# Kernel tuning notes

Measured on AMD Instinct MI355X. Metric: run time of the kernel, lower is better.

## Reference

```python
import jax, jax.numpy as jnp
import numpy as np

N_NODES = 50000
N_EDGES = 1600000
N_GRAPHS = 64


def gcn_conv(x, edge_index, W, b):
    """GCNConv: out = D^{-1/2} (A + I) D^{-1/2} X W + b (symmetric norm, self-loops)."""
    n = x.shape[0]
    src = jnp.concatenate([edge_index[0], jnp.arange(n)])  # add self-loops
    dst = jnp.concatenate([edge_index[1], jnp.arange(n)])
    deg = jax.ops.segment_sum(jnp.ones_like(dst, dtype=x.dtype), dst, num_segments=n)
    dinv = jax.lax.rsqrt(jnp.maximum(deg, 1.0))
    norm = dinv[src] * dinv[dst]                      # [E+N]
    h = x @ W                                          # transform first (smaller gather)
    msg = norm[:, None] * h[src]                       # [E+N, out_dim]
    out = jax.ops.segment_sum(msg, dst, num_segments=n)
    return out + b


def global_mean_pool(x, batch, num_graphs):
    s = jax.ops.segment_sum(x, batch, num_segments=num_graphs)
    cnt = jax.ops.segment_sum(jnp.ones((x.shape[0],), x.dtype), batch, num_segments=num_graphs)
    return s / jnp.maximum(cnt, 1.0)[:, None]


def setup_inputs() -> dict:
    key = jax.random.key(0)
    ks = jax.random.split(key, 6)
    x = jax.random.normal(ks[0], (N_NODES, 256), dtype=jnp.float32)
    edge_index = jax.random.randint(ks[1], (2, N_EDGES), 0, N_NODES, dtype=jnp.int64)
    batch = jnp.sort(jax.random.randint(ks[2], (N_NODES,), 0, N_GRAPHS, dtype=jnp.int64))
    W1 = jax.random.normal(ks[3], (256, 256), dtype=jnp.float32) * (1.0 / np.sqrt(256))
    b1 = jnp.zeros((256,), jnp.float32)
    W2 = jax.random.normal(ks[4], (256, 10), dtype=jnp.float32) * (1.0 / np.sqrt(256))
    b2 = jnp.zeros((10,), jnp.float32)
    return {"x": x, "edge_index": edge_index, "batch": batch,
            "W1": W1, "b1": b1, "W2": W2, "b2": b2}


def reference(x, edge_index, batch, W1, b1, W2, b2):
    h = gcn_conv(x, edge_index, W1, b1)
    h = jax.nn.elu(h)
    # dropout: identity (inference mode, training=False)
    h = gcn_conv(h, edge_index, W2, b2)
    h = jax.nn.elu(h)
    g = global_mean_pool(h, batch, N_GRAPHS)          # [num_graphs, num_class]
    return jax.nn.log_softmax(g, axis=-1)
```

## Files before the change

### kernel.cpp

```cpp
#include <hip/hip_runtime.h>
#include <hip/hip_bf16.h>
#include <math.h>

typedef unsigned int uint;
typedef unsigned short ushort;

typedef __attribute__((ext_vector_type(8))) short bf16x8;
typedef __attribute__((ext_vector_type(4))) float f32x4;

__device__ __forceinline__ float bf2f(uint u) {
    return __uint_as_float(u << 16);
}
__device__ __forceinline__ ushort f2bf(float f) {
    uint u = __float_as_uint(f);
    uint rounding = 0x7fffu + ((u >> 16) & 1u);
    return (ushort)((u + rounding) >> 16);
}
__device__ __forceinline__ float elu(float x) {
    return x > 0.f ? x : expm1f(x);
}

__global__ void count_kernel(const int* __restrict__ dst, int E, int* __restrict__ cnt) {
    int i = blockIdx.x * blockDim.x + threadIdx.x;
    int stride = gridDim.x * blockDim.x;
    for (; i < E; i += stride) atomicAdd(&cnt[dst[i]], 1);
}

__global__ void scan1_kernel(const int* __restrict__ cnt, int NN, int* __restrict__ partials) {
    __shared__ int sh[256];
    int i = blockIdx.x * 256 + threadIdx.x;
    sh[threadIdx.x] = (i < NN) ? cnt[i] : 0;
    __syncthreads();
    for (int s = 128; s > 0; s >>= 1) {
        if (threadIdx.x < s) sh[threadIdx.x] += sh[threadIdx.x + s];
        __syncthreads();
    }
    if (threadIdx.x == 0) partials[blockIdx.x] = sh[0];
}

__global__ void scan2_kernel(const int* __restrict__ partials, int nb, int* __restrict__ pscan) {
    if (threadIdx.x == 0) {
        int run = 0;
        for (int b = 0; b < nb; ++b) { pscan[b] = run; run += partials[b]; }
    }
}

__global__ void scan3_kernel(const int* __restrict__ cnt, int NN, const int* __restrict__ pscan,
                             int* __restrict__ offs, int* __restrict__ cursor,
                             float* __restrict__ dinv) {
    __shared__ int sh[256];
    int t = threadIdx.x;
    int i = blockIdx.x * 256 + t;
    int v = (i < NN) ? cnt[i] : 0;
    sh[t] = v;
    __syncthreads();
    for (int d = 1; d < 256; d <<= 1) {
        int x = (t >= d) ? sh[t - d] : 0;
        __syncthreads();
        sh[t] += x;
        __syncthreads();
    }
    int incl = sh[t];
    int excl = incl - v;
    int base = pscan[blockIdx.x];
    if (i < NN) {
        offs[i]   = base + excl;
        cursor[i] = base + excl;
        dinv[i]   = rsqrtf((float)v + 1.0f);
        if (i == NN - 1) offs[NN] = base + incl;
    }
}

__global__ __launch_bounds__(256) void scatter_kernel(const int* __restrict__ src,
                                                      const int* __restrict__ dst, int E,
                                                      int* __restrict__ cursor,
                                                      int* __restrict__ ssrc, int NN) {
    int grp = blockIdx.x & 7;
    int per = (NN + 7) >> 3;
    int lo = grp * per;
    int hi = min(NN, lo + per);
    int bid = blockIdx.x >> 3;
    int nb  = gridDim.x >> 3;
    int i = bid * blockDim.x + threadIdx.x;
    int stride = nb * blockDim.x;
    for (; i < E; i += stride) {
        int d = dst[i];
        if (d >= lo && d < hi) {
            int pos = atomicAdd(&cursor[d], 1);
            ssrc[pos] = src[i];
        }
    }
}

__global__ void gstart_kernel(const int* __restrict__ batch, int NN, int NG,
                              int* __restrict__ gstart) {
    int g = blockIdx.x * blockDim.x + threadIdx.x;
    if (g > NG) return;
    int lo = 0, hi = NN;
    while (lo < hi) {
        int mid = (lo + hi) >> 1;
        if (batch[mid] < g) lo = mid + 1; else hi = mid;
    }
    gstart[g] = lo;
}

__global__ __launch_bounds__(256) void wtrans_kernel(const float* __restrict__ W,
                                                     ushort* __restrict__ WT) {
    __shared__ float T[64][68];
    int b = blockIdx.x;
    int kt = (b >> 2) * 64, nt = (b & 3) * 64;
    int t = threadIdx.x;
    int r = t >> 4, c4 = (t & 15) * 4;
    #pragma unroll
    for (int h = 0; h < 4; ++h) {
        int rr = r + h * 16;
        float4 v = *reinterpret_cast<const float4*>(&W[(size_t)(kt + rr) * 256 + nt + c4]);
        *reinterpret_cast<float4*>(&T[rr][c4]) = v;
    }
    __syncthreads();
    int nr = t >> 2, ks = (t & 3) * 16;
    uint o[8];
    #pragma unroll
    for (int i = 0; i < 16; i += 2) {
        float f0 = T[ks + i][nr];
        float f1 = T[ks + i + 1][nr];
        o[i >> 1] = (uint)f2bf(f0) | ((uint)f2bf(f1) << 16);
    }
    size_t base = (size_t)(nt + nr) * 256 + kt + ks;
    *reinterpret_cast<uint4*>(&WT[base])     = make_uint4(o[0], o[1], o[2], o[3]);
    *reinterpret_cast<uint4*>(&WT[base + 8]) = make_uint4(o[4], o[5], o[6], o[7]);
}

#define G1_STRIDE 40
__global__ __launch_bounds__(256) void gemm1_mfma_kernel(const float* __restrict__ X,
                                                         const ushort* __restrict__ W1T,
                                                         const float* __restrict__ dinv,
                                                         ushort* __restrict__ H1, int M) {
    __shared__ ushort Xs[64 * G1_STRIDE];
    __shared__ ushort Ws[256 * G1_STRIDE];
    __shared__ float  Dvs[64];
    int t = threadIdx.x;
    int row0 = blockIdx.x * 64;
    int lane = t & 63;
    int w = t >> 6;
    int lr = lane & 15;
    int lg = lane >> 4;

    if (t < 64) {
        int grow = row0 + t;
        Dvs[t] = (grow < M) ? dinv[grow] : 0.f;
    }

    f32x4 acc[4][4];
    #pragma unroll
    for (int j = 0; j < 4; ++j)
        #pragma unroll
        for (int i = 0; i < 4; ++i)
            acc[j][i] = (f32x4){0.f, 0.f, 0.f, 0.f};

    for (int k0 = 0; k0 < 256; k0 += 32) {
        #pragma unroll
        for (int h = 0; h < 2; ++h) {
            int u = t + h * 256;
            int row = u >> 3;
            int kq = (u & 7) * 4;
            int grow = row0 + row;
            float4 v = make_float4(0.f, 0.f, 0.f, 0.f);
            if (grow < M) v = *reinterpret_cast<const float4*>(&X[(size_t)grow * 256 + k0 + kq]);
            uint lo = (uint)f2bf(v.x) | ((uint)f2bf(v.y) << 16);
            uint hi = (uint)f2bf(v.z) | ((uint)f2bf(v.w) << 16);
            *reinterpret_cast<uint2*>(&Xs[row * G1_STRIDE + kq]) = make_uint2(lo, hi);
        }
        #pragma unroll
        for (int h = 0; h < 4; ++h) {
            int u = t + h * 256;
            int n = u >> 2;
            int seg = u & 3;
            uint4 wv = *reinterpret_cast<const uint4*>(&W1T[(size_t)n * 256 + k0 + seg * 8]);
            *reinterpret_cast<uint4*>(&Ws[n * G1_STRIDE + seg * 8]) = wv;
        }
        __syncthreads();
        bf16x8 wf[4], xf[4];
        #pragma unroll
        for (int j = 0; j < 4; ++j)
            wf[j] = *reinterpret_cast<const bf16x8*>(&Ws[(w * 64 + j * 16 + lr) * G1_STRIDE + lg * 8]);
        #pragma unroll
        for (int i = 0; i < 4; ++i)
            xf[i] = *reinterpret_cast<const bf16x8*>(&Xs[(i * 16 + lr) * G1_STRIDE + lg * 8]);
        #pragma unroll
        for (int j = 0; j < 4; ++j)
            #pragma unroll
            for (int i = 0; i < 4; ++i)
                acc[j][i] = __builtin_amdgcn_mfma_f32_16x16x32_bf16(wf[j], xf[i], acc[j][i], 0, 0, 0);
        __syncthreads();
    }

    #pragma unroll
    for (int mi = 0; mi < 4; ++mi) {
        int grow = row0 + mi * 16 + lr;
        float dv = Dvs[mi * 16 + lr];
        bool ok = grow < M;
        #pragma unroll
        for (int nj = 0; nj < 4; ++nj) {
            f32x4 a = acc[nj][mi];
            uint lo = (uint)f2bf(a[0] * dv) | ((uint)f2bf(a[1] * dv) << 16);
            uint hi = (uint)f2bf(a[2] * dv) | ((uint)f2bf(a[3] * dv) << 16);
            if (ok) {
                int col = w * 64 + nj * 16 + lg * 4;
                *reinterpret_cast<uint2*>(&H1[(size_t)grow * 256 + col]) = make_uint2(lo, hi);
            }
        }
    }
}

__global__ __launch_bounds__(256) void agg1_gemm2_kernel(
    const ushort* __restrict__ H1, const int* __restrict__ offs, const int* __restrict__ ssrc,
    const float* __restrict__ dinv, const float* __restrict__ b1, const float* __restrict__ W2,
    float* __restrict__ H2, int NN) {
    int lane = threadIdx.x & 63;
    int node = blockIdx.x * 4 + (threadIdx.x >> 6);
    if (node >= NN) return;
    int beg = offs[node], end = offs[node + 1];
    int col = lane * 4;
    const ushort* H1c = H1 + col;
    float acc0 = 0.f, acc1 = 0.f, acc2 = 0.f, acc3 = 0.f;
    int i = beg;
    for (; i + 3 < end; i += 4) {
        int s0 = ssrc[i], s1 = ssrc[i + 1], s2 = ssrc[i + 2], s3 = ssrc[i + 3];
        uint2 p0 = *reinterpret_cast<const uint2*>(H1c + (size_t)s0 * 256);
        uint2 p1 = *reinterpret_cast<const uint2*>(H1c + (size_t)s1 * 256);
        uint2 p2 = *reinterpret_cast<const uint2*>(H1c + (size_t)s2 * 256);
        uint2 p3 = *reinterpret_cast<const uint2*>(H1c + (size_t)s3 * 256);
        acc0 += bf2f(p0.x & 0xffffu) + bf2f(p1.x & 0xffffu) + bf2f(p2.x & 0xffffu) + bf2f(p3.x & 0xffffu);
        acc1 += bf2f(p0.x >> 16)     + bf2f(p1.x >> 16)     + bf2f(p2.x >> 16)     + bf2f(p3.x >> 16);
        acc2 += bf2f(p0.y & 0xffffu) + bf2f(p1.y & 0xffffu) + bf2f(p2.y & 0xffffu) + bf2f(p3.y & 0xffffu);
        acc3 += bf2f(p0.y >> 16)     + bf2f(p1.y >> 16)     + bf2f(p2.y >> 16)     + bf2f(p3.y >> 16);
    }
    for (; i < end; ++i) {
        int s = ssrc[i];
        uint2 p = *reinterpret_cast<const uint2*>(H1c + (size_t)s * 256);
        acc0 += bf2f(p.x & 0xffffu);
        acc1 += bf2f(p.x >> 16);
        acc2 += bf2f(p.y & 0xffffu);
        acc3 += bf2f(p.y >> 16);
    }
    {
        uint2 p = *reinterpret_cast<const uint2*>(H1c + (size_t)node * 256);
        acc0 += bf2f(p.x & 0xffffu);
        acc1 += bf2f(p.x >> 16);
        acc2 += bf2f(p.y & 0xffffu);
        acc3 += bf2f(p.y >> 16);
    }
    float dn = dinv[node];
    float a0 = elu(fmaf(acc0, dn, b1[col + 0]));
    float a1 = elu(fmaf(acc1, dn, b1[col + 1]));
    float a2 = elu(fmaf(acc2, dn, b1[col + 2]));
    float a3 = elu(fmaf(acc3, dn, b1[col + 3]));
    float hv = 0.f;
    #pragma unroll
    for (int c = 0; c < 10; ++c) {
        float p = a0 * W2[(col + 0) * 10 + c]
                + a1 * W2[(col + 1) * 10 + c]
                + a2 * W2[(col + 2) * 10 + c]
                + a3 * W2[(col + 3) * 10 + c];
        #pragma unroll
        for (int m = 1; m < 64; m <<= 1) p += __shfl_xor(p, m, 64);
        if (lane == c) hv = p;
    }
    if (lane < 10) H2[(size_t)node * 10 + lane] = dn * hv;
}

__global__ __launch_bounds__(256) void agg2_elu_kernel(
    const float* __restrict__ H2, const int* __restrict__ offs, const int* __restrict__ ssrc,
    const float* __restrict__ dinv, const float* __restrict__ b2,
    float* __restrict__ H2act, int NN) {
    int t = threadIdx.x;
    int node = blockIdx.x * 8 + (t >> 5);
    if (node >= NN) return;
    int sub = t & 31;
    int c = sub & 15;
    int e2 = sub >> 4;
    int beg = offs[node], end = offs[node + 1];
    float acc = 0.f;
    int i = beg + e2;
    for (; i + 6 < end; i += 8) {
        int s0 = ssrc[i], s1 = ssrc[i + 2], s2 = ssrc[i + 4], s3 = ssrc[i + 6];
        float h0 = H2[(size_t)s0 * 10 + c];
        float h1 = H2[(size_t)s1 * 10 + c];
        float h2 = H2[(size_t)s2 * 10 + c];
        float h3 = H2[(size_t)s3 * 10 + c];
        acc += (h0 + h1) + (h2 + h3);
    }
    for (; i < end; i += 2) acc += H2[(size_t)ssrc[i] * 10 + c];
    if (e2 == 0) acc += H2[(size_t)node * 10 + c];
    acc += __shfl_xor(acc, 16, 64);
    if (sub < 10) {
        float dn = dinv[node];
        H2act[(size_t)node * 10 + c] = elu(fmaf(dn, acc, b2[c]));
    }
}

__global__ __launch_bounds__(320) void pool_final_kernel(
    const float* __restrict__ H2act, const int* __restrict__ gstart,
    float* __restrict__ out, int NG) {
    __shared__ float red[32][10];
    __shared__ float m[10];
    __shared__ float s_lse;
    int g = blockIdx.x;
    int t = threadIdx.x;
    int grp = t / 10;
    int c = t - grp * 10;
    int lo = gstart[g], hi = gstart[g + 1];
    float acc = 0.f;
    if (grp < 32) {
        for (int n = lo + grp; n < hi; n += 32) acc += H2act[(size_t)n * 10 + c];
        red[grp][c] = acc;
    }
    __syncthreads();
    if (t < 10) {
        float s = 0.f;
        #pragma unroll
        for (int j = 0; j < 32; ++j) s += red[j][t];
        m[t] = s / fmaxf((float)(hi - lo), 1.0f);
    }
    __syncthreads();
    if (t == 0) {
        float mx = -1e30f;
        for (int c2 = 0; c2 < 10; ++c2) mx = fmaxf(mx, m[c2]);
        float s = 0.f;
        for (int c2 = 0; c2 < 10; ++c2) s += expf(m[c2] - mx);
        s_lse = logf(s) + mx;
    }
    __syncthreads();
    if (t < 10) out[g * 10 + t] = m[t] - s_lse;
}

extern "C" void kernel_launch(void* const* d_in, const int* in_sizes, int n_in,
                              void* d_out, int out_size, void* d_ws, size_t ws_size,
                              hipStream_t stream) {
    const float* x     = (const float*)d_in[0];
    const int*   eidx  = (const int*)d_in[1];
    const int*   batch = (const int*)d_in[2];
    const float* W1    = (const float*)d_in[3];
    const float* b1    = (const float*)d_in[4];
    const float* W2    = (const float*)d_in[5];
    const float* b2    = (const float*)d_in[6];

    int NN = in_sizes[0] / 256;
    int E  = in_sizes[1] / 2;
    int NG = out_size / 10;
    const int* src = eidx;
    const int* dst = eidx + E;

    char* ws = (char*)d_ws;
    size_t off = 0;
    auto alloc = [&](size_t bytes) -> void* {
        void* p = ws + off;
        off += (bytes + 255) & ~((size_t)255);
        return p;
    };
    int*    cnt      = (int*)alloc((size_t)NN * 4);
    int*    offs     = (int*)alloc((size_t)(NN + 1) * 4);
    int*    cursor   = (int*)alloc((size_t)NN * 4);
    int*    partials = (int*)alloc(256 * 4);
    int*    pscan    = (int*)alloc(256 * 4);
    float*  dinv     = (float*)alloc((size_t)NN * 4);
    int*    gstart   = (int*)alloc((size_t)(NG + 1) * 4);
    ushort* W1T      = (ushort*)alloc((size_t)256 * 256 * 2);
    int*    ssrc     = (int*)alloc((size_t)E * 4);
    ushort* H1       = (ushort*)alloc((size_t)NN * 256 * 2);
    float*  H2       = (float*)alloc((size_t)NN * 10 * 4);
    float*  H2act    = (float*)alloc((size_t)NN * 10 * 4);

    hipMemsetAsync(cnt, 0, (size_t)NN * 4, stream);

    int nb = (NN + 255) / 256;
    count_kernel  <<<1024, 256, 0, stream>>>(dst, E, cnt);
    scan1_kernel  <<<nb, 256, 0, stream>>>(cnt, NN, partials);
    scan2_kernel  <<<1, 64, 0, stream>>>(partials, nb, pscan);
    scan3_kernel  <<<nb, 256, 0, stream>>>(cnt, NN, pscan, offs, cursor, dinv);
    scatter_kernel<<<2048, 256, 0, stream>>>(src, dst, E, cursor, ssrc, NN);
    gstart_kernel <<<1, 128, 0, stream>>>(batch, NN, NG, gstart);
    wtrans_kernel <<<16, 256, 0, stream>>>(W1, W1T);
    gemm1_mfma_kernel<<<(NN + 63) / 64, 256, 0, stream>>>(x, W1T, dinv, H1, NN);
    agg1_gemm2_kernel<<<(NN + 3) / 4, 256, 0, stream>>>(H1, offs, ssrc, dinv, b1, W2, H2, NN);
    agg2_elu_kernel  <<<(NN + 7) / 8, 256, 0, stream>>>(H2, offs, ssrc, dinv, b2, H2act, NN);
    pool_final_kernel<<<NG, 320, 0, stream>>>(H2act, gstart, (float*)d_out, NG);
}
```

Before: 352.6 us.

## Split layer-1 aggregation into column-sliced gather kernel and separate GEMM2 kernel

```diff
diff --git a/kernel.cpp b/kernel.cpp
--- a/kernel.cpp
+++ b/kernel.cpp
@@ -10,6 +10,12 @@
 
 __device__ __forceinline__ float bf2f(uint u) {
     return __uint_as_float(u << 16);
+}
+__device__ __forceinline__ float bf2f_lo(uint u) {
+    return __uint_as_float(u << 16);
+}
+__device__ __forceinline__ float bf2f_hi(uint u) {
+    return __uint_as_float(u & 0xffff0000u);
 }
 __device__ __forceinline__ ushort f2bf(float f) {
     uint u = __float_as_uint(f);
@@ -213,61 +219,88 @@
     }
 }
 
-__global__ __launch_bounds__(256) void agg1_gemm2_kernel(
+__global__ __launch_bounds__(256) void agg1_slice_kernel(
     const ushort* __restrict__ H1, const int* __restrict__ offs, const int* __restrict__ ssrc,
-    const float* __restrict__ dinv, const float* __restrict__ b1, const float* __restrict__ W2,
+    const float* __restrict__ dinv, const float* __restrict__ b1,
+    ushort* __restrict__ A1, int NN) {
+    int g = blockIdx.x & 7;
+    int node = (blockIdx.x >> 3) * 4 + (threadIdx.x >> 6);
+    if (node >= NN) return;
+    int lane = threadIdx.x & 63;
+    int e = lane >> 3;
+    int f = lane & 7;
+    int c0 = g * 32 + f * 4;
+    const ushort* H1c = H1 + c0;
+    int beg = offs[node], end = offs[node + 1];
+    float acc0 = 0.f, acc1 = 0.f, acc2 = 0.f, acc3 = 0.f;
+    int i = beg + e;
+    for (; i + 8 < end; i += 16) {
+        int s0 = ssrc[i], s1 = ssrc[i + 8];
+        uint2 p0 = *reinterpret_cast<const uint2*>(H1c + (size_t)s0 * 256);
+        uint2 p1 = *reinterpret_cast<const uint2*>(H1c + (size_t)s1 * 256);
+        acc0 += bf2f_lo(p0.x) + bf2f_lo(p1.x);
+        acc1 += bf2f_hi(p0.x) + bf2f_hi(p1.x);
+        acc2 += bf2f_lo(p0.y) + bf2f_lo(p1.y);
+        acc3 += bf2f_hi(p0.y) + bf2f_hi(p1.y);
+    }
+    for (; i < end; i += 8) {
+        int s = ssrc[i];
+        uint2 p = *reinterpret_cast<const uint2*>(H1c + (size_t)s * 256);
+        acc0 += bf2f_lo(p.x);
+        acc1 += bf2f_hi(p.x);
+        acc2 += bf2f_lo(p.y);
+        acc3 += bf2f_hi(p.y);
+    }
+    if (e == 0) {
+        uint2 p = *reinterpret_cast<const uint2*>(H1c + (size_t)node * 256);
+        acc0 += bf2f_lo(p.x);
+        acc1 += bf2f_hi(p.x);
+        acc2 += bf2f_lo(p.y);
+        acc3 += bf2f_hi(p.y);
+    }
+    #pragma unroll
+    for (int m = 8; m < 64; m <<= 1) {
+        acc0 += __shfl_xor(acc0, m, 64);
+        acc1 += __shfl_xor(acc1, m, 64);
+        acc2 += __shfl_xor(acc2, m, 64);
+        acc3 += __shfl_xor(acc3, m, 64);
+    }
+    if (e == 0) {
+        float dn = dinv[node];
+        float a0 = elu(fmaf(acc0, dn, b1[c0 + 0]));
+        float a1 = elu(fmaf(acc1, dn, b1[c0 + 1]));
+        float a2 = elu(fmaf(acc2, dn, b1[c0 + 2]));
+        float a3 = elu(fmaf(acc3, dn, b1[c0 + 3]));
+        uint lo = (uint)f2bf(a0) | ((uint)f2bf(a1) << 16);
+        uint hi = (uint)f2bf(a2) | ((uint)f2bf(a3) << 16);
+        *reinterpret_cast<uint2*>(&A1[(size_t)node * 256 + c0]) = make_uint2(lo, hi);
+    }
+}
+
+__global__ __launch_bounds__(256) void gemm2_kernel(
+    const ushort* __restrict__ A1, const float* __restrict__ dinv, const float* __restrict__ W2,
     float* __restrict__ H2, int NN) {
     int lane = threadIdx.x & 63;
     int node = blockIdx.x * 4 + (threadIdx.x >> 6);
     if (node >= NN) return;
-    int beg = offs[node], end = offs[node + 1];
     int col = lane * 4;
-    const ushort* H1c = H1 + col;
-    float acc0 = 0.f, acc1 = 0.f, acc2 = 0.f, acc3 = 0.f;
-    int i = beg;
-    for (; i + 3 < end; i += 4) {
-        int s0 = ssrc[i], s1 = ssrc[i + 1], s2 = ssrc[i + 2], s3 = ssrc[i + 3];
-        uint2 p0 = *reinterpret_cast<const uint2*>(H1c + (size_t)s0 * 256);
-        uint2 p1 = *reinterpret_cast<const uint2*>(H1c + (size_t)s1 * 256);
-        uint2 p2 = *reinterpret_cast<const uint2*>(H1c + (size_t)s2 * 256);
-        uint2 p3 = *reinterpret_cast<const uint2*>(H1c + (size_t)s3 * 256);
-        acc0 += bf2f(p0.x & 0xffffu) + bf2f(p1.x & 0xffffu) + bf2f(p2.x & 0xffffu) + bf2f(p3.x & 0xffffu);
-        acc1 += bf2f(p0.x >> 16)     + bf2f(p1.x >> 16)     + bf2f(p2.x >> 16)     + bf2f(p3.x >> 16);
-        acc2 += bf2f(p0.y & 0xffffu) + bf2f(p1.y & 0xffffu) + bf2f(p2.y & 0xffffu) + bf2f(p3.y & 0xffffu);
-        acc3 += bf2f(p0.y >> 16)     + bf2f(p1.y >> 16)     + bf2f(p2.y >> 16)     + bf2f(p3.y >> 16);
-    }
-    for (; i < end; ++i) {
-        int s = ssrc[i];
-        uint2 p = *reinterpret_cast<const uint2*>(H1c + (size_t)s * 256);
-        acc0 += bf2f(p.x & 0xffffu);
-        acc1 += bf2f(p.x >> 16);
-        acc2 += bf2f(p.y & 0xffffu);
-        acc3 += bf2f(p.y >> 16);
-    }
-    {
-        uint2 p = *reinterpret_cast<const uint2*>(H1c + (size_t)node * 256);
-        acc0 += bf2f(p.x & 0xffffu);
-        acc1 += bf2f(p.x >> 16);
-        acc2 += bf2f(p.y & 0xffffu);
-        acc3 += bf2f(p.y >> 16);
-    }
-    float dn = dinv[node];
-    float a0 = elu(fmaf(acc0, dn, b1[col + 0]));
-    float a1 = elu(fmaf(acc1, dn, b1[col + 1]));
-    float a2 = elu(fmaf(acc2, dn, b1[col + 2]));
-    float a3 = elu(fmaf(acc3, dn, b1[col + 3]));
+    uint2 p = *reinterpret_cast<const uint2*>(&A1[(size_t)node * 256 + col]);
+    float a0 = bf2f_lo(p.x);
+    float a1 = bf2f_hi(p.x);
+    float a2 = bf2f_lo(p.y);
+    float a3 = bf2f_hi(p.y);
     float hv = 0.f;
     #pragma unroll
     for (int c = 0; c < 10; ++c) {
-        float p = a0 * W2[(col + 0) * 10 + c]
+        float q = a0 * W2[(col + 0) * 10 + c]
                 + a1 * W2[(col + 1) * 10 + c]
                 + a2 * W2[(col + 2) * 10 + c]
                 + a3 * W2[(col + 3) * 10 + c];
         #pragma unroll
-        for (int m = 1; m < 64; m <<= 1) p += __shfl_xor(p, m, 64);
-        if (lane == c) hv = p;
-    }
-    if (lane < 10) H2[(size_t)node * 10 + lane] = dn * hv;
+        for (int m = 1; m < 64; m <<= 1) q += __shfl_xor(q, m, 64);
+        if (lane == c) hv = q;
+    }
+    if (lane < 10) H2[(size_t)node * 10 + lane] = dinv[node] * hv;
 }
 
 __global__ __launch_bounds__(256) void agg2_elu_kernel(
@@ -369,6 +402,7 @@
     ushort* W1T      = (ushort*)alloc((size_t)256 * 256 * 2);
     int*    ssrc     = (int*)alloc((size_t)E * 4);
     ushort* H1       = (ushort*)alloc((size_t)NN * 256 * 2);
+    ushort* A1       = (ushort*)alloc((size_t)NN * 256 * 2);
     float*  H2       = (float*)alloc((size_t)NN * 10 * 4);
     float*  H2act    = (float*)alloc((size_t)NN * 10 * 4);
 
@@ -383,7 +417,8 @@
     gstart_kernel <<<1, 128, 0, stream>>>(batch, NN, NG, gstart);
     wtrans_kernel <<<16, 256, 0, stream>>>(W1, W1T);
     gemm1_mfma_kernel<<<(NN + 63) / 64, 256, 0, stream>>>(x, W1T, dinv, H1, NN);
-    agg1_gemm2_kernel<<<(NN + 3) / 4, 256, 0, stream>>>(H1, offs, ssrc, dinv, b1, W2, H2, NN);
+    agg1_slice_kernel<<<((NN + 3) / 4) * 8, 256, 0, stream>>>(H1, offs, ssrc, dinv, b1, A1, NN);
+    gemm2_kernel     <<<(NN + 3) / 4, 256, 0, stream>>>(A1, dinv, W2, H2, NN);
     agg2_elu_kernel  <<<(NN + 7) / 8, 256, 0, stream>>>(H2, offs, ssrc, dinv, b2, H2act, NN);
     pool_final_kernel<<<NG, 320, 0, stream>>>(H2act, gstart, (float*)d_out, NG);
 }
```

After: 511.0 us. +44.9%, slower.

## Bucket CSR neighbor lists by source block for gather locality

Applied to the files above, without the earlier changes.

```diff
diff --git a/kernel.cpp b/kernel.cpp
--- a/kernel.cpp
+++ b/kernel.cpp
@@ -8,8 +8,14 @@
 typedef __attribute__((ext_vector_type(8))) short bf16x8;
 typedef __attribute__((ext_vector_type(4))) float f32x4;
 
-__device__ __forceinline__ float bf2f(uint u) {
+#define SBLK_SHIFT 12
+#define SBLK_STRIDE 16
+
+__device__ __forceinline__ float bf2f_lo(uint u) {
     return __uint_as_float(u << 16);
+}
+__device__ __forceinline__ float bf2f_hi(uint u) {
+    return __uint_as_float(u & 0xffff0000u);
 }
 __device__ __forceinline__ ushort f2bf(float f) {
     uint u = __float_as_uint(f);
@@ -20,16 +26,18 @@
     return x > 0.f ? x : expm1f(x);
 }
 
-__global__ void count_kernel(const int* __restrict__ dst, int E, int* __restrict__ cnt) {
+__global__ void count2_kernel(const int* __restrict__ src, const int* __restrict__ dst, int E,
+                              int* __restrict__ cnt2) {
     int i = blockIdx.x * blockDim.x + threadIdx.x;
     int stride = gridDim.x * blockDim.x;
-    for (; i < E; i += stride) atomicAdd(&cnt[dst[i]], 1);
-}
-
-__global__ void scan1_kernel(const int* __restrict__ cnt, int NN, int* __restrict__ partials) {
+    for (; i < E; i += stride)
+        atomicAdd(&cnt2[dst[i] * SBLK_STRIDE + (src[i] >> SBLK_SHIFT)], 1);
+}
+
+__global__ void scan1_kernel(const int* __restrict__ cnt, int M, int* __restrict__ partials) {
     __shared__ int sh[256];
     int i = blockIdx.x * 256 + threadIdx.x;
-    sh[threadIdx.x] = (i < NN) ? cnt[i] : 0;
+    sh[threadIdx.x] = (i < M) ? cnt[i] : 0;
     __syncthreads();
     for (int s = 128; s > 0; s >>= 1) {
         if (threadIdx.x < s) sh[threadIdx.x] += sh[threadIdx.x + s];
@@ -38,20 +46,41 @@
     if (threadIdx.x == 0) partials[blockIdx.x] = sh[0];
 }
 
-__global__ void scan2_kernel(const int* __restrict__ partials, int nb, int* __restrict__ pscan) {
-    if (threadIdx.x == 0) {
-        int run = 0;
-        for (int b = 0; b < nb; ++b) { pscan[b] = run; run += partials[b]; }
-    }
-}
-
-__global__ void scan3_kernel(const int* __restrict__ cnt, int NN, const int* __restrict__ pscan,
-                             int* __restrict__ offs, int* __restrict__ cursor,
-                             float* __restrict__ dinv) {
+__global__ __launch_bounds__(256) void scan2_kernel(const int* __restrict__ partials, int nb,
+                                                    int* __restrict__ pscan) {
+    __shared__ int tsum[256];
+    int t = threadIdx.x;
+    int pref[16];
+    int s = 0;
+    #pragma unroll
+    for (int j = 0; j < 16; ++j) {
+        int idx = t * 16 + j;
+        int v = (idx < nb) ? partials[idx] : 0;
+        pref[j] = s;
+        s += v;
+    }
+    tsum[t] = s;
+    __syncthreads();
+    for (int d = 1; d < 256; d <<= 1) {
+        int x = (t >= d) ? tsum[t - d] : 0;
+        __syncthreads();
+        tsum[t] += x;
+        __syncthreads();
+    }
+    int base = (t == 0) ? 0 : tsum[t - 1];
+    #pragma unroll
+    for (int j = 0; j < 16; ++j) {
+        int idx = t * 16 + j;
+        if (idx < nb) pscan[idx] = base + pref[j];
+    }
+}
+
+__global__ void scan3_kernel(const int* __restrict__ cnt, int M, const int* __restrict__ pscan,
+                             int* __restrict__ offs2, int* __restrict__ cursor2) {
     __shared__ int sh[256];
     int t = threadIdx.x;
     int i = blockIdx.x * 256 + t;
-    int v = (i < NN) ? cnt[i] : 0;
+    int v = (i < M) ? cnt[i] : 0;
     sh[t] = v;
     __syncthreads();
     for (int d = 1; d < 256; d <<= 1) {
@@ -60,20 +89,28 @@
         sh[t] += x;
         __syncthreads();
     }
-    int incl = sh[t];
-    int excl = incl - v;
+    int excl = sh[t] - v;
     int base = pscan[blockIdx.x];
-    if (i < NN) {
-        offs[i]   = base + excl;
-        cursor[i] = base + excl;
-        dinv[i]   = rsqrtf((float)v + 1.0f);
-        if (i == NN - 1) offs[NN] = base + incl;
-    }
+    if (i < M) {
+        offs2[i]   = base + excl;
+        cursor2[i] = base + excl;
+    }
+}
+
+__global__ void post_kernel(const int* __restrict__ offs2, int NN, int E,
+                            int* __restrict__ offs, float* __restrict__ dinv) {
+    int n = blockIdx.x * blockDim.x + threadIdx.x;
+    if (n >= NN) return;
+    int o = offs2[n * SBLK_STRIDE];
+    int nxt = (n == NN - 1) ? E : offs2[(n + 1) * SBLK_STRIDE];
+    offs[n] = o;
+    dinv[n] = rsqrtf((float)(nxt - o) + 1.0f);
+    if (n == NN - 1) offs[NN] = E;
 }
 
 __global__ __launch_bounds__(256) void scatter_kernel(const int* __restrict__ src,
                                                       const int* __restrict__ dst, int E,
-                                                      int* __restrict__ cursor,
+                                                      int* __restrict__ cursor2,
                                                       int* __restrict__ ssrc, int NN) {
     int grp = blockIdx.x & 7;
     int per = (NN + 7) >> 3;
@@ -86,8 +123,9 @@
     for (; i < E; i += stride) {
         int d = dst[i];
         if (d >= lo && d < hi) {
-            int pos = atomicAdd(&cursor[d], 1);
-            ssrc[pos] = src[i];
+            int s = src[i];
+            int pos = atomicAdd(&cursor2[d * SBLK_STRIDE + (s >> SBLK_SHIFT)], 1);
+            ssrc[pos] = s;
         }
     }
 }
@@ -231,25 +269,25 @@
         uint2 p1 = *reinterpret_cast<const uint2*>(H1c + (size_t)s1 * 256);
         uint2 p2 = *reinterpret_cast<const uint2*>(H1c + (size_t)s2 * 256);
         uint2 p3 = *reinterpret_cast<const uint2*>(H1c + (size_t)s3 * 256);
-        acc0 += bf2f(p0.x & 0xffffu) + bf2f(p1.x & 0xffffu) + bf2f(p2.x & 0xffffu) + bf2f(p3.x & 0xffffu);
-        acc1 += bf2f(p0.x >> 16)     + bf2f(p1.x >> 16)     + bf2f(p2.x >> 16)     + bf2f(p3.x >> 16);
-        acc2 += bf2f(p0.y & 0xffffu) + bf2f(p1.y & 0xffffu) + bf2f(p2.y & 0xffffu) + bf2f(p3.y & 0xffffu);
-        acc3 += bf2f(p0.y >> 16)     + bf2f(p1.y >> 16)     + bf2f(p2.y >> 16)     + bf2f(p3.y >> 16);
+        acc0 += bf2f_lo(p0.x) + bf2f_lo(p1.x) + bf2f_lo(p2.x) + bf2f_lo(p3.x);
+        acc1 += bf2f_hi(p0.x) + bf2f_hi(p1.x) + bf2f_hi(p2.x) + bf2f_hi(p3.x);
+        acc2 += bf2f_lo(p0.y) + bf2f_lo(p1.y) + bf2f_lo(p2.y) + bf2f_lo(p3.y);
+        acc3 += bf2f_hi(p0.y) + bf2f_hi(p1.y) + bf2f_hi(p2.y) + bf2f_hi(p3.y);
     }
     for (; i < end; ++i) {
         int s = ssrc[i];
         uint2 p = *reinterpret_cast<const uint2*>(H1c + (size_t)s * 256);
-        acc0 += bf2f(p.x & 0xffffu);
-        acc1 += bf2f(p.x >> 16);
-        acc2 += bf2f(p.y & 0xffffu);
-        acc3 += bf2f(p.y >> 16);
+        acc0 += bf2f_lo(p.x);
+        acc1 += bf2f_hi(p.x);
+        acc2 += bf2f_lo(p.y);
+        acc3 += bf2f_hi(p.y);
     }
     {
         uint2 p = *reinterpret_cast<const uint2*>(H1c + (size_t)node * 256);
-        acc0 += bf2f(p.x & 0xffffu);
-        acc1 += bf2f(p.x >> 16);
-        acc2 += bf2f(p.y & 0xffffu);
-        acc3 += bf2f(p.y >> 16);
+        acc0 += bf2f_lo(p.x);
+        acc1 += bf2f_hi(p.x);
+        acc2 += bf2f_lo(p.y);
+        acc3 += bf2f_hi(p.y);
     }
     float dn = dinv[node];
     float a0 = elu(fmaf(acc0, dn, b1[col + 0]));
@@ -352,6 +390,8 @@
     const int* src = eidx;
     const int* dst = eidx + E;
 
+    int M2 = NN * SBLK_STRIDE;
+
     char* ws = (char*)d_ws;
     size_t off = 0;
     auto alloc = [&](size_t bytes) -> void* {
@@ -359,11 +399,12 @@
         off += (bytes + 255) & ~((size_t)255);
         return p;
     };
-    int*    cnt      = (int*)alloc((size_t)NN * 4);
+    int*    cnt2     = (int*)alloc((size_t)M2 * 4);
+    int*    offs2    = (int*)alloc((size_t)M2 * 4);
+    int*    cursor2  = (int*)alloc((size_t)M2 * 4);
     int*    offs     = (int*)alloc((size_t)(NN + 1) * 4);
-    int*    cursor   = (int*)alloc((size_t)NN * 4);
-    int*    partials = (int*)alloc(256 * 4);
-    int*    pscan    = (int*)alloc(256 * 4);
+    int*    partials = (int*)alloc(4096 * 4);
+    int*    pscan    = (int*)alloc(4096 * 4);
     float*  dinv     = (float*)alloc((size_t)NN * 4);
     int*    gstart   = (int*)alloc((size_t)(NG + 1) * 4);
     ushort* W1T      = (ushort*)alloc((size_t)256 * 256 * 2);
@@ -372,14 +413,15 @@
     float*  H2       = (float*)alloc((size_t)NN * 10 * 4);
     float*  H2act    = (float*)alloc((size_t)NN * 10 * 4);
 
-    hipMemsetAsync(cnt, 0, (size_t)NN * 4, stream);
-
-    int nb = (NN + 255) / 256;
-    count_kernel  <<<1024, 256, 0, stream>>>(dst, E, cnt);
-    scan1_kernel  <<<nb, 256, 0, stream>>>(cnt, NN, partials);
-    scan2_kernel  <<<1, 64, 0, stream>>>(partials, nb, pscan);
-    scan3_kernel  <<<nb, 256, 0, stream>>>(cnt, NN, pscan, offs, cursor, dinv);
-    scatter_kernel<<<2048, 256, 0, stream>>>(src, dst, E, cursor, ssrc, NN);
+    hipMemsetAsync(cnt2, 0, (size_t)M2 * 4, stream);
+
+    int nb2 = (M2 + 255) / 256;
+    count2_kernel <<<1024, 256, 0, stream>>>(src, dst, E, cnt2);
+    scan1_kernel  <<<nb2, 256, 0, stream>>>(cnt2, M2, partials);
+    scan2_kernel  <<<1, 256, 0, stream>>>(partials, nb2, pscan);
+    scan3_kernel  <<<nb2, 256, 0, stream>>>(cnt2, M2, pscan, offs2, cursor2);
+    post_kernel   <<<(NN + 255) / 256, 256, 0, stream>>>(offs2, NN, E, offs, dinv);
+    scatter_kernel<<<2048, 256, 0, stream>>>(src, dst, E, cursor2, ssrc, NN);
     gstart_kernel <<<1, 128, 0, stream>>>(batch, NN, NG, gstart);
     wtrans_kernel <<<16, 256, 0, stream>>>(W1, W1T);
     gemm1_mfma_kernel<<<(NN + 63) / 64, 256, 0, stream>>>(x, W1T, dinv, H1, NN);
```

Measured after the change: 337.4 us. 4.3% less time.
